# Performance work log

Hardware: AMD Instinct MI355X
Metric: run time of the kernel (lower is better)

Reference implementation:

```python
import jax, jax.numpy as jnp
import numpy as np

N_NODES = 50000
N_EDGES = 800000
DIM = 128
HEADS = 2
DEPTH = 2
MLP = 512
NEG_SLOPE = 0.2  # PyG GATv2 default
EPS = 1e-5


def setup_inputs() -> dict:
    key = jax.random.key(0)
    ks = jax.random.split(key, 10)
    s = 0.05
    p = lambda k, shape: (jax.random.normal(k, shape, jnp.float32) * s)
    x = jax.random.normal(ks[0], (N_NODES, DIM), jnp.float32)
    edge_index = jax.random.randint(ks[1], (2, N_EDGES), 0, N_NODES, dtype=jnp.int64)
    D, H = DEPTH, HEADS
    return {
        "x": x,
        "edge_index": edge_index,
        # per-layer stacked params (leading dim = depth)
        "ln1_g": jnp.ones((D, DIM), jnp.float32), "ln1_b": jnp.zeros((D, DIM), jnp.float32),
        "Wl": p(ks[2], (D, DIM, H * DIM)), "bl": jnp.zeros((D, H * DIM), jnp.float32),
        "Wr": p(ks[3], (D, DIM, H * DIM)), "br": jnp.zeros((D, H * DIM), jnp.float32),
        "att": p(ks[4], (D, H, DIM)),
        "gat_b": jnp.zeros((D, H * DIM), jnp.float32),
        "proj_W": p(ks[5], (D, H * DIM, DIM)), "proj_b": jnp.zeros((D, DIM), jnp.float32),
        "ln2_g": jnp.ones((D, DIM), jnp.float32), "ln2_b": jnp.zeros((D, DIM), jnp.float32),
        "W1": p(ks[6], (D, DIM, MLP)), "b1": jnp.zeros((D, MLP), jnp.float32),
        "W2": p(ks[7], (D, MLP, DIM)), "b2": jnp.zeros((D, DIM), jnp.float32),
    }


def _layer_norm(x, g, b):
    m = jnp.mean(x, axis=-1, keepdims=True)
    v = jnp.var(x, axis=-1, keepdims=True)
    return (x - m) * jax.lax.rsqrt(v + EPS) * g + b


def _gatv2(x, src, dst, Wl, bl, Wr, br, att, gat_b):
    # GATv2Conv: e_ij = att^T LeakyReLU(Wl x_j + Wr x_i); alpha = segment-softmax over dst
    n = x.shape[0]
    xl = (x @ Wl + bl).reshape(n, HEADS, DIM)  # source transform [N,H,D]
    xr = (x @ Wr + br).reshape(n, HEADS, DIM)  # target transform [N,H,D]
    e = jax.nn.leaky_relu(xl[src] + xr[dst], NEG_SLOPE)      # [E,H,D]
    score = jnp.einsum('ehd,hd->eh', e, att)                 # [E,H]
    smax = jax.ops.segment_max(score, dst, num_segments=n)   # [N,H]
    ex = jnp.exp(score - smax[dst])
    denom = jax.ops.segment_sum(ex, dst, num_segments=n)     # [N,H]
    alpha = ex / (denom[dst] + 1e-16)                        # [E,H]
    msg = xl[src] * alpha[..., None]                         # [E,H,D]
    out = jax.ops.segment_sum(msg, dst, num_segments=n)      # [N,H,D]
    return out.reshape(n, HEADS * DIM) + gat_b


def reference(x, edge_index, ln1_g, ln1_b, Wl, bl, Wr, br, att, gat_b,
              proj_W, proj_b, ln2_g, ln2_b, W1, b1, W2, b2):
    src, dst = edge_index[0], edge_index[1]
    for i in range(DEPTH):
        h = _layer_norm(x, ln1_g[i], ln1_b[i])               # PreNorm
        g = _gatv2(h, src, dst, Wl[i], bl[i], Wr[i], br[i], att[i], gat_b[i])
        x = x + (g @ proj_W[i] + proj_b[i])                  # QuickFix proj + Residual
        h = _layer_norm(x, ln2_g[i], ln2_b[i])
        x = x + (jax.nn.gelu(h @ W1[i] + b1[i]) @ W2[i] + b2[i])  # FFN + Residual
    return x
```

## Files before the change

### kernel.cpp

```cpp
#include <hip/hip_runtime.h>

typedef unsigned int uint;
typedef unsigned short ushort;
typedef __attribute__((ext_vector_type(4))) float f32x4;
typedef __attribute__((ext_vector_type(2))) float f32x2;
typedef __attribute__((ext_vector_type(8))) short bf16x8;
typedef _Float16 f16x2 __attribute__((ext_vector_type(2)));

#define N_NODES 50000
#define DIM 128
#define HEADS 2
#define HD 256
#define MLP 512
#define DEPTH 2
#define CAP 96

__device__ __forceinline__ uint f2bf(float f) {
    uint u = __float_as_uint(f);
    return (u + 0x7FFFu + ((u >> 16) & 1u)) >> 16;
}
__device__ __forceinline__ ushort f2h(float f) {
    union { _Float16 h; ushort u; } v;
    v.h = (_Float16)f;
    return v.u;
}
__device__ __forceinline__ f16x2 u2h(uint u) {
    union { uint u; f16x2 h; } v;
    v.u = u;
    return v.h;
}

#if __has_builtin(__builtin_amdgcn_fdot2)
#define FDOT2(a, b, c) __builtin_amdgcn_fdot2((a), (b), (c), false)
#else
#define FDOT2(a, b, c) fmaf((float)(a)[0], (float)(b)[0], fmaf((float)(a)[1], (float)(b)[1], (c)))
#endif
#if __has_builtin(__builtin_amdgcn_exp2f)
#define EXP2F(x) __builtin_amdgcn_exp2f(x)
#else
#define EXP2F(x) exp2f(x)
#endif

__device__ __forceinline__ float gelu_tanh(float x) {
    float t = 0.7978845608028654f * (x + 0.044715f * x * x * x);
    float e = __expf(2.0f * t);
    float th = 1.0f - 2.0f / (e + 1.0f);
    return 0.5f * x * (1.0f + th);
}

__global__ __launch_bounds__(256) void ln_kernel(
    const float* __restrict__ x, const float* __restrict__ g,
    const float* __restrict__ b, ushort* __restrict__ out, int N)
{
    int node = blockIdx.x * 4 + (threadIdx.x >> 6);
    if (node >= N) return;
    int lane = threadIdx.x & 63;
    const float2 v = *(const float2*)(x + (size_t)node * DIM + lane * 2);
    float s = v.x + v.y;
    float s2 = v.x * v.x + v.y * v.y;
    #pragma unroll
    for (int m = 1; m <= 32; m <<= 1) {
        s  += __shfl_xor(s,  m, 64);
        s2 += __shfl_xor(s2, m, 64);
    }
    float mean = s * (1.0f / 128.0f);
    float var  = s2 * (1.0f / 128.0f) - mean * mean;
    float rs = rsqrtf(var + 1e-5f);
    float ox = (v.x - mean) * rs * g[lane * 2]     + b[lane * 2];
    float oy = (v.y - mean) * rs * g[lane * 2 + 1] + b[lane * 2 + 1];
    uint pk = f2bf(ox) | (f2bf(oy) << 16);
    *(uint*)(out + (size_t)node * DIM + lane * 2) = pk;
}

__global__ __launch_bounds__(256) void wconv_all(
    const float* __restrict__ Wl, const float* __restrict__ Wr,
    const float* __restrict__ pW, const float* __restrict__ W1,
    const float* __restrict__ W2, ushort* __restrict__ WlWr_t,
    ushort* __restrict__ pW_t, ushort* __restrict__ W1_t,
    ushort* __restrict__ W2_t)
{
    int i = blockIdx.x * 256 + threadIdx.x;
    if (i < 65536) {
        int l = i >> 15, rem = i & 32767;
        int k = rem >> 8, m = rem & 255;
        WlWr_t[l * 65536 + m * 128 + k] = (ushort)f2bf(Wl[i]);
    } else if (i < 131072) {
        int j = i - 65536;
        int l = j >> 15, rem = j & 32767;
        int k = rem >> 8, m = rem & 255;
        WlWr_t[l * 65536 + (m + 256) * 128 + k] = (ushort)f2bf(Wr[j]);
    } else if (i < 196608) {
        int j = i - 131072;
        int l = j >> 15, rem = j & 32767;
        int k = rem >> 7, m = rem & 127;
        pW_t[l * 32768 + m * 256 + k] = (ushort)f2bf(pW[j]);
    } else if (i < 327680) {
        int j = i - 196608;
        int l = j >> 16, rem = j & 65535;
        int k = rem >> 9, m = rem & 511;
        W1_t[l * 65536 + m * 128 + k] = (ushort)f2bf(W1[j]);
    } else if (i < 458752) {
        int j = i - 327680;
        int l = j >> 16, rem = j & 65535;
        int k = rem >> 7, m = rem & 127;
        W2_t[l * 65536 + m * 512 + k] = (ushort)f2bf(W2[j]);
    }
}

template<int EPI>
__global__ __launch_bounds__(256) void gemm_mfma(
    const ushort* __restrict__ A, const ushort* __restrict__ Bt,
    const float* __restrict__ bias, const float* __restrict__ bias2, int bsplit,
    void* __restrict__ Cout, int Nr, int K, int M)
{
    __shared__ ushort As[128 * 72];
    __shared__ ushort Bs[64 * 72];
    const int tid = threadIdx.x;
    const int wave = tid >> 6, lane = tid & 63;
    const int wm = wave >> 1, wn = wave & 1;
    const int r0 = blockIdx.y * 128;
    const int c0 = blockIdx.x * 64;
    const int l15 = lane & 15, q = lane >> 4;

    f32x4 acc[4][2];
    #pragma unroll
    for (int t = 0; t < 4; ++t)
        #pragma unroll
        for (int u = 0; u < 2; ++u) {
            f32x4 z = {0.f, 0.f, 0.f, 0.f};
            acc[t][u] = z;
        }

    for (int k0 = 0; k0 < K; k0 += 64) {
        #pragma unroll
        for (int p = 0; p < 4; ++p) {
            int flat = p * 256 + tid;
            int row = flat >> 3, c8 = flat & 7;
            int gr = r0 + row; gr = gr < Nr ? gr : Nr - 1;
            uint4 v = *(const uint4*)(A + (size_t)gr * K + k0 + c8 * 8);
            *(uint4*)(As + row * 72 + c8 * 8) = v;
        }
        #pragma unroll
        for (int p = 0; p < 2; ++p) {
            int flat = p * 256 + tid;
            int row = flat >> 3, c8 = flat & 7;
            uint4 v = *(const uint4*)(Bt + (size_t)(c0 + row) * K + k0 + c8 * 8);
            *(uint4*)(Bs + row * 72 + c8 * 8) = v;
        }
        __syncthreads();
        #pragma unroll
        for (int kh = 0; kh < 2; ++kh) {
            const int ko = kh * 32 + q * 8;
            bf16x8 a[4], b[2];
            #pragma unroll
            for (int t = 0; t < 4; ++t)
                a[t] = *(const bf16x8*)(As + (wm * 64 + t * 16 + l15) * 72 + ko);
            #pragma unroll
            for (int u = 0; u < 2; ++u)
                b[u] = *(const bf16x8*)(Bs + (wn * 32 + u * 16 + l15) * 72 + ko);
            #pragma unroll
            for (int t = 0; t < 4; ++t)
                #pragma unroll
                for (int u = 0; u < 2; ++u)
                    acc[t][u] = __builtin_amdgcn_mfma_f32_16x16x32_bf16(
                        a[t], b[u], acc[t][u], 0, 0, 0);
        }
        __syncthreads();
    }

    #pragma unroll
    for (int t = 0; t < 4; ++t) {
        int grow = r0 + wm * 64 + t * 16 + q * 4;
        #pragma unroll
        for (int u = 0; u < 2; ++u) {
            int gcol = c0 + wn * 32 + u * 16 + l15;
            float bv = (gcol < bsplit) ? bias[gcol] : bias2[gcol - bsplit];
            #pragma unroll
            for (int i = 0; i < 4; ++i) {
                int r = grow + i;
                if (r >= Nr) continue;
                float v = acc[t][u][i] + bv;
                if (EPI == 1) v = gelu_tanh(v);
                if (EPI == 0) {
                    ((ushort*)Cout)[(size_t)r * M + gcol] = f2h(v);
                } else {
                    ((ushort*)Cout)[(size_t)r * M + gcol] = (ushort)f2bf(v);
                }
            }
        }
    }
}

__global__ __launch_bounds__(256) void gemm_ln(
    const ushort* __restrict__ A, const ushort* __restrict__ Bt,
    const float* __restrict__ bias, const float* __restrict__ R,
    float* __restrict__ X, const float* __restrict__ lng,
    const float* __restrict__ lnb, ushort* __restrict__ H,
    int Nr, int K)
{
    __shared__ ushort As[64 * 72];
    __shared__ ushort Bs[128 * 72];
    __shared__ float4 part[64];
    const int tid = threadIdx.x;
    const int wave = tid >> 6, lane = tid & 63;
    const int wm = wave >> 1, wn = wave & 1;
    const int r0 = blockIdx.y * 64;
    const int l15 = lane & 15, q = lane >> 4;

    f32x4 acc[2][4];
    #pragma unroll
    for (int t = 0; t < 2; ++t)
        #pragma unroll
        for (int u = 0; u < 4; ++u) {
            f32x4 z = {0.f, 0.f, 0.f, 0.f};
            acc[t][u] = z;
        }

    for (int k0 = 0; k0 < K; k0 += 64) {
        #pragma unroll
        for (int p = 0; p < 2; ++p) {
            int flat = p * 256 + tid;
            int row = flat >> 3, c8 = flat & 7;
            int gr = r0 + row; gr = gr < Nr ? gr : Nr - 1;
            uint4 v = *(const uint4*)(A + (size_t)gr * K + k0 + c8 * 8);
            *(uint4*)(As + row * 72 + c8 * 8) = v;
        }
        #pragma unroll
        for (int p = 0; p < 4; ++p) {
            int flat = p * 256 + tid;
            int row = flat >> 3, c8 = flat & 7;
            uint4 v = *(const uint4*)(Bt + (size_t)row * K + k0 + c8 * 8);
            *(uint4*)(Bs + row * 72 + c8 * 8) = v;
        }
        __syncthreads();
        #pragma unroll
        for (int kh = 0; kh < 2; ++kh) {
            const int ko = kh * 32 + q * 8;
            bf16x8 a[2], b[4];
            #pragma unroll
            for (int t = 0; t < 2; ++t)
                a[t] = *(const bf16x8*)(As + (wm * 32 + t * 16 + l15) * 72 + ko);
            #pragma unroll
            for (int u = 0; u < 4; ++u)
                b[u] = *(const bf16x8*)(Bs + (wn * 64 + u * 16 + l15) * 72 + ko);
            #pragma unroll
            for (int t = 0; t < 2; ++t)
                #pragma unroll
                for (int u = 0; u < 4; ++u)
                    acc[t][u] = __builtin_amdgcn_mfma_f32_16x16x32_bf16(
                        a[t], b[u], acc[t][u], 0, 0, 0);
        }
        __syncthreads();
    }

    float bv[4];
    #pragma unroll
    for (int u = 0; u < 4; ++u) bv[u] = bias[wn * 64 + u * 16 + l15];

    #pragma unroll
    for (int t = 0; t < 2; ++t) {
        #pragma unroll
        for (int i = 0; i < 4; ++i) {
            const int rl = wm * 32 + t * 16 + q * 4 + i;
            const int r = r0 + rl;
            const bool ok = r < Nr;
            float ss = 0.f, ss2 = 0.f;
            #pragma unroll
            for (int u = 0; u < 4; ++u) {
                const int col = wn * 64 + u * 16 + l15;
                float v = acc[t][u][i] + bv[u];
                if (ok) v += R[(size_t)r * DIM + col];
                acc[t][u][i] = v;
                ss += v; ss2 += v * v;
            }
            #pragma unroll
            for (int m = 1; m <= 8; m <<= 1) {
                ss  += __shfl_xor(ss,  m, 64);
                ss2 += __shfl_xor(ss2, m, 64);
            }
            if (ok) {
                #pragma unroll
                for (int u = 0; u < 4; ++u)
                    X[(size_t)r * DIM + wn * 64 + u * 16 + l15] = acc[t][u][i];
            }
            if (l15 == 0) {
                float2 w = { ss, ss2 };
                *(float2*)((float*)&part[rl] + wn * 2) = w;
            }
        }
    }

    if (H != nullptr) {
        __syncthreads();
        float lgv[4], lbv[4];
        #pragma unroll
        for (int u = 0; u < 4; ++u) {
            lgv[u] = lng[wn * 64 + u * 16 + l15];
            lbv[u] = lnb[wn * 64 + u * 16 + l15];
        }
        #pragma unroll
        for (int t = 0; t < 2; ++t) {
            #pragma unroll
            for (int i = 0; i < 4; ++i) {
                const int rl = wm * 32 + t * 16 + q * 4 + i;
                const int r = r0 + rl;
                if (r >= Nr) continue;
                const float4 pp = part[rl];
                const float mean = (pp.x + pp.z) * (1.0f / 128.0f);
                const float var  = (pp.y + pp.w) * (1.0f / 128.0f) - mean * mean;
                const float rs = rsqrtf(var + 1e-5f);
                #pragma unroll
                for (int u = 0; u < 4; ++u) {
                    const int col = wn * 64 + u * 16 + l15;
                    const float hv = (acc[t][u][i] - mean) * rs * lgv[u] + lbv[u];
                    H[(size_t)r * DIM + col] = (ushort)f2bf(hv);
                }
            }
        }
    }
}

__global__ __launch_bounds__(256) void bucket_kernel(
    const int* __restrict__ src, const int* __restrict__ dst,
    int* __restrict__ deg, ushort* __restrict__ esrc, int E)
{
    int e = blockIdx.x * 256 + threadIdx.x;
    if (e >= E) return;
    int d = dst[e];
    int pos = atomicAdd(&deg[d], 1);
    if (pos < CAP) esrc[(size_t)d * CAP + pos] = (ushort)src[e];
}

__global__ __launch_bounds__(256) void gat_gather(
    const int* __restrict__ deg, const ushort* __restrict__ esrc,
    const ushort* __restrict__ xlr, const float* __restrict__ att,
    const float* __restrict__ gat_b, ushort* __restrict__ agg, int N)
{
    int node = blockIdx.x * 4 + (threadIdx.x >> 6);
    if (node >= N) return;
    const int lane = threadIdx.x & 63;
    const int half = lane >> 5, sl = lane & 31;
    const int c = sl * 8;

    const uint4 rq = *(const uint4*)(xlr + (size_t)node * 512 + 256 + c);
    const f16x2 r01 = u2h(rq.x), r23 = u2h(rq.y);
    const f16x2 r45 = u2h(rq.z), r67 = u2h(rq.w);

    const float LOG2E = 1.4426950408889634f;
    const float4 af0 = *(const float4*)(att + c);
    const float4 af1 = *(const float4*)(att + c + 4);
    f16x2 a01, a23, a45, a67;
    a01[0] = (_Float16)(af0.x * LOG2E); a01[1] = (_Float16)(af0.y * LOG2E);
    a23[0] = (_Float16)(af0.z * LOG2E); a23[1] = (_Float16)(af0.w * LOG2E);
    a45[0] = (_Float16)(af1.x * LOG2E); a45[1] = (_Float16)(af1.y * LOG2E);
    a67[0] = (_Float16)(af1.z * LOG2E); a67[1] = (_Float16)(af1.w * LOG2E);
    const f16x2 k02 = { (_Float16)0.2f, (_Float16)0.2f };

    int dc = deg[node]; dc = dc < CAP ? dc : CAP;
    const int base = node * CAP;
    f32x2 acc01 = {0.f, 0.f}, acc23 = {0.f, 0.f}, acc45 = {0.f, 0.f}, acc67 = {0.f, 0.f};
    float den = 0.f;

    if (dc > 0) {
        int slc = sl < dc ? sl : dc - 1;
        const int idxreg = esrc[base + slc];

        auto getsrc = [&](int e) -> int {
            int idx = e < dc ? e : dc - 1;
            int s = __shfl(idxreg, (lane & 32) | (idx & 31), 64);
            if (idx >= 32) s = esrc[base + idx];
            return s;
        };

        const int iters = (dc + 1) >> 1;
        int e0 = half;
        int s0 = getsrc(e0);
        uint4 lq0 = *(const uint4*)(xlr + (size_t)s0 * 512 + c);
        int e1 = e0 + 2;
        int s1 = getsrc(e1);
        uint4 lq1 = *(const uint4*)(xlr + (size_t)s1 * 512 + c);

        for (int it = 0; it < iters; ++it) {
            const int e2 = e0 + 4;
            const int s2 = getsrc(e2);
            const uint4 lq2 = *(const uint4*)(xlr + (size_t)s2 * 512 + c);

            const f16x2 l01 = u2h(lq0.x), l23 = u2h(lq0.y);
            const f16x2 l45 = u2h(lq0.z), l67 = u2h(lq0.w);
            f16x2 t, lr;
            float p = 0.f;
            t = l01 + r01; lr = __builtin_elementwise_max(t, t * k02); p = FDOT2(a01, lr, p);
            t = l23 + r23; lr = __builtin_elementwise_max(t, t * k02); p = FDOT2(a23, lr, p);
            t = l45 + r45; lr = __builtin_elementwise_max(t, t * k02); p = FDOT2(a45, lr, p);
            t = l67 + r67; lr = __builtin_elementwise_max(t, t * k02); p = FDOT2(a67, lr, p);
            p += __shfl_xor(p, 1, 64);
            p += __shfl_xor(p, 2, 64);
            p += __shfl_xor(p, 4, 64);
            p += __shfl_xor(p, 8, 64);
            const float ex = (e0 < dc) ? EXP2F(p) : 0.f;
            acc01.x = fmaf(ex, (float)l01[0], acc01.x);
            acc01.y = fmaf(ex, (float)l01[1], acc01.y);
            acc23.x = fmaf(ex, (float)l23[0], acc23.x);
            acc23.y = fmaf(ex, (float)l23[1], acc23.y);
            acc45.x = fmaf(ex, (float)l45[0], acc45.x);
            acc45.y = fmaf(ex, (float)l45[1], acc45.y);
            acc67.x = fmaf(ex, (float)l67[0], acc67.x);
            acc67.y = fmaf(ex, (float)l67[1], acc67.y);
            den += ex;
            e0 = e1; lq0 = lq1;
            e1 = e2; lq1 = lq2;
        }
    }
    acc01.x += __shfl_xor(acc01.x, 32, 64); acc01.y += __shfl_xor(acc01.y, 32, 64);
    acc23.x += __shfl_xor(acc23.x, 32, 64); acc23.y += __shfl_xor(acc23.y, 32, 64);
    acc45.x += __shfl_xor(acc45.x, 32, 64); acc45.y += __shfl_xor(acc45.y, 32, 64);
    acc67.x += __shfl_xor(acc67.x, 32, 64); acc67.y += __shfl_xor(acc67.y, 32, 64);
    den     += __shfl_xor(den,     32, 64);

    if (half == 0) {
        const float inv = 1.0f / (den + 1e-16f);
        const float4 g0 = *(const float4*)(gat_b + c);
        const float4 g1 = *(const float4*)(gat_b + c + 4);
        uint4 o;
        o.x = f2bf(acc01.x * inv + g0.x) | (f2bf(acc01.y * inv + g0.y) << 16);
        o.y = f2bf(acc23.x * inv + g0.z) | (f2bf(acc23.y * inv + g0.w) << 16);
        o.z = f2bf(acc45.x * inv + g1.x) | (f2bf(acc45.y * inv + g1.y) << 16);
        o.w = f2bf(acc67.x * inv + g1.z) | (f2bf(acc67.y * inv + g1.w) << 16);
        *(uint4*)(agg + (size_t)node * HD + c) = o;
    }
}

extern "C" void kernel_launch(void* const* d_in, const int* in_sizes, int n_in,
                              void* d_out, int out_size, void* d_ws, size_t ws_size,
                              hipStream_t stream) {
    const float* x_in   = (const float*)d_in[0];
    const int*   eidx   = (const int*)d_in[1];
    const float* ln1_g  = (const float*)d_in[2];
    const float* ln1_b  = (const float*)d_in[3];
    const float* Wl     = (const float*)d_in[4];
    const float* bl     = (const float*)d_in[5];
    const float* Wr     = (const float*)d_in[6];
    const float* br     = (const float*)d_in[7];
    const float* att    = (const float*)d_in[8];
    const float* gat_b  = (const float*)d_in[9];
    const float* projW  = (const float*)d_in[10];
    const float* projb  = (const float*)d_in[11];
    const float* ln2_g  = (const float*)d_in[12];
    const float* ln2_b  = (const float*)d_in[13];
    const float* W1     = (const float*)d_in[14];
    const float* b1     = (const float*)d_in[15];
    const float* W2     = (const float*)d_in[16];
    const float* b2     = (const float*)d_in[17];

    const int N = N_NODES;
    const int E = in_sizes[1] / 2;
    const int* src = eidx;
    const int* dst = eidx + E;

    char* ws = (char*)d_ws;
    size_t off = 0;
    ushort* xlr  = (ushort*)(ws + off); off += (size_t)N * 512 * 2;
    ushort* agg  = (ushort*)(ws + off); off += (size_t)N * HD * 2;
    ushort* h    = (ushort*)(ws + off); off += (size_t)N * DIM * 2;
    ushort* WlWr_t = (ushort*)(ws + off); off += (size_t)DEPTH * 512 * 128 * 2;
    ushort* pW_t   = (ushort*)(ws + off); off += (size_t)DEPTH * 128 * 256 * 2;
    ushort* W1_t   = (ushort*)(ws + off); off += (size_t)DEPTH * 512 * 128 * 2;
    ushort* W2_t   = (ushort*)(ws + off); off += (size_t)DEPTH * 128 * 512 * 2;
    int* deg     = (int*)(ws + off);    off += (size_t)N * 4;
    ushort* esrc = (ushort*)(ws + off); off += (size_t)N * CAP * 2;
    ushort* mid  = xlr;

    float* x = (float*)d_out;

    const int nodeBlocks = (N + 3) / 4;
    const dim3 blk(256);
    const int gy128 = (N + 127) / 128;
    const int gy64  = (N + 63) / 64;

    wconv_all<<<(458752 + 255) / 256, blk, 0, stream>>>(
        Wl, Wr, projW, W1, W2, WlWr_t, pW_t, W1_t, W2_t);

    hipMemsetAsync(deg, 0, (size_t)N * 4, stream);
    bucket_kernel<<<(E + 255) / 256, blk, 0, stream>>>(src, dst, deg, esrc, E);

    for (int L = 0; L < DEPTH; ++L) {
        const float* bl_i   = bl + (size_t)L * HD;
        const float* br_i   = br + (size_t)L * HD;
        const float* att_i  = att + (size_t)L * HD;
        const float* gatb_i = gat_b + (size_t)L * HD;
        const float* pb_i   = projb + (size_t)L * DIM;
        const float* b1_i   = b1 + (size_t)L * MLP;
        const float* b2_i   = b2 + (size_t)L * DIM;
        const float* xin_L  = (L == 0) ? x_in : x;

        if (L == 0)
            ln_kernel<<<nodeBlocks, blk, 0, stream>>>(
                x_in, ln1_g, ln1_b, h, N);

        gemm_mfma<0><<<dim3(8, gy128), blk, 0, stream>>>(
            h, WlWr_t + (size_t)L * 512 * 128, bl_i, br_i, HD, xlr, N, 128, 512);
        gat_gather<<<nodeBlocks, blk, 0, stream>>>(deg, esrc, xlr, att_i, gatb_i, agg, N);
        gemm_ln<<<dim3(1, gy64), blk, 0, stream>>>(
            agg, pW_t + (size_t)L * 128 * 256, pb_i, xin_L, x,
            ln2_g + (size_t)L * DIM, ln2_b + (size_t)L * DIM, h, N, 256);
        gemm_mfma<1><<<dim3(8, gy128), blk, 0, stream>>>(
            h, W1_t + (size_t)L * 512 * 128, b1_i, b1_i, 1 << 30, mid, N, 128, 512);
        const bool last = (L + 1 == DEPTH);
        gemm_ln<<<dim3(1, gy64), blk, 0, stream>>>(
            mid, W2_t + (size_t)L * 128 * 512, b2_i, x, x,
            last ? nullptr : ln1_g + (size_t)(L + 1) * DIM,
            last ? nullptr : ln1_b + (size_t)(L + 1) * DIM,
            last ? nullptr : h, N, 512);
    }
}
```

Measured before the change: 540.3 us.

## Fuse FFN up-projection, GELU and down-projection into one kernel

Replaces the separate W1 GEMM (writing a 512-wide bf16 intermediate to global memory) and the W2 GEMM+LN kernel with a single kernel. It keeps each 32-row tile's GELU output in shared memory and feeds it straight into the second MFMA GEMM, then does the residual and the next LayerNorm. W2 is stored with its K index permuted so the packed-pair layout in shared memory lines up with MFMA operand order. The goal is to drop the intermediate global write and read plus one launch. In exchange, weights are read directly from global memory per block without LDS staging, and each block carries a larger shared-memory footprint.

```diff
diff --git a/kernel.cpp b/kernel.cpp
--- a/kernel.cpp
+++ b/kernel.cpp
@@ -103,7 +103,11 @@
         int j = i - 327680;
         int l = j >> 16, rem = j & 65535;
         int k = rem >> 7, m = rem & 127;
-        W2_t[l * 65536 + m * 512 + k] = (ushort)f2bf(W2[j]);
+        int nc = k >> 6, r64 = k & 63;
+        int w = r64 >> 5, r32 = r64 & 31;
+        int hf = r32 >> 4, lo = r32 & 15;
+        int ks = nc * 64 + ((w * 16 + lo) << 1) + hf;
+        W2_t[l * 65536 + m * 512 + ks] = (ushort)f2bf(W2[j]);
     }
 }
 
@@ -315,6 +319,137 @@
                     const float hv = (acc[t][u][i] - mean) * rs * lgv[u] + lbv[u];
                     H[(size_t)r * DIM + col] = (ushort)f2bf(hv);
                 }
+            }
+        }
+    }
+}
+
+__global__ __launch_bounds__(256) void ffn_fused(
+    const ushort* __restrict__ h, const ushort* __restrict__ W1t,
+    const ushort* __restrict__ W2tp, const float* __restrict__ b1,
+    const float* __restrict__ b2, const float* __restrict__ R,
+    float* __restrict__ X, const float* __restrict__ lng,
+    const float* __restrict__ lnb, ushort* __restrict__ H, int Nr)
+{
+    __shared__ ushort As[32 * 140];
+    __shared__ uint  mid[32 * 259];
+    __shared__ float4 part[32];
+    const int tid = threadIdx.x;
+    const int wave = tid >> 6, lane = tid & 63;
+    const int wm = wave >> 1, wn = wave & 1;
+    const int l15 = lane & 15, q = lane >> 4;
+    const int r0 = blockIdx.x * 32;
+
+    #pragma unroll
+    for (int p = 0; p < 2; ++p) {
+        int f = p * 256 + tid;
+        int row = f >> 4, c8 = f & 15;
+        int gr = r0 + row; gr = gr < Nr ? gr : Nr - 1;
+        uint4 v = *(const uint4*)(h + (size_t)gr * DIM + c8 * 8);
+        *(uint4*)(As + row * 140 + c8 * 8) = v;
+    }
+    __syncthreads();
+
+    bf16x8 af[4];
+    #pragma unroll
+    for (int ks = 0; ks < 4; ++ks)
+        af[ks] = *(const bf16x8*)(As + (wm * 16 + l15) * 140 + ks * 32 + q * 8);
+
+    #pragma unroll
+    for (int nc = 0; nc < 8; ++nc) {
+        f32x4 pa[2];
+        #pragma unroll
+        for (int u = 0; u < 2; ++u) { f32x4 z = {0.f,0.f,0.f,0.f}; pa[u] = z; }
+        #pragma unroll
+        for (int u = 0; u < 2; ++u) {
+            const ushort* bp = W1t + (size_t)(nc * 64 + wn * 32 + u * 16 + l15) * 128 + q * 8;
+            #pragma unroll
+            for (int ks = 0; ks < 4; ++ks) {
+                bf16x8 b = *(const bf16x8*)(bp + ks * 32);
+                pa[u] = __builtin_amdgcn_mfma_f32_16x16x32_bf16(af[ks], b, pa[u], 0, 0, 0);
+            }
+        }
+        const float bv0 = b1[nc * 64 + wn * 32 + l15];
+        const float bv1 = b1[nc * 64 + wn * 32 + 16 + l15];
+        #pragma unroll
+        for (int i = 0; i < 4; ++i) {
+            float v0 = gelu_tanh(pa[0][i] + bv0);
+            float v1 = gelu_tanh(pa[1][i] + bv1);
+            mid[(wm * 16 + q * 4 + i) * 259 + nc * 32 + wn * 16 + l15] =
+                f2bf(v0) | (f2bf(v1) << 16);
+        }
+    }
+    __syncthreads();
+
+    f32x4 acc[4];
+    #pragma unroll
+    for (int u = 0; u < 4; ++u) { f32x4 z = {0.f,0.f,0.f,0.f}; acc[u] = z; }
+    #pragma unroll
+    for (int ks = 0; ks < 16; ++ks) {
+        bf16x8 a = *(const bf16x8*)(mid + (wm * 16 + l15) * 259 + ks * 16 + q * 4);
+        #pragma unroll
+        for (int u = 0; u < 4; ++u) {
+            bf16x8 b = *(const bf16x8*)(W2tp + (size_t)(wn * 64 + u * 16 + l15) * 512 + ks * 32 + q * 8);
+            acc[u] = __builtin_amdgcn_mfma_f32_16x16x32_bf16(a, b, acc[u], 0, 0, 0);
+        }
+    }
+
+    float bvv[4];
+    #pragma unroll
+    for (int u = 0; u < 4; ++u) bvv[u] = b2[wn * 64 + u * 16 + l15];
+
+    #pragma unroll
+    for (int i = 0; i < 4; ++i) {
+        const int rl = wm * 16 + q * 4 + i;
+        const int r = r0 + rl;
+        const bool ok = r < Nr;
+        float ss = 0.f, ss2 = 0.f;
+        #pragma unroll
+        for (int u = 0; u < 4; ++u) {
+            const int col = wn * 64 + u * 16 + l15;
+            float v = acc[u][i] + bvv[u];
+            if (ok) v += R[(size_t)r * DIM + col];
+            acc[u][i] = v;
+            ss += v; ss2 += v * v;
+        }
+        #pragma unroll
+        for (int m = 1; m <= 8; m <<= 1) {
+            ss  += __shfl_xor(ss,  m, 64);
+            ss2 += __shfl_xor(ss2, m, 64);
+        }
+        if (ok) {
+            #pragma unroll
+            for (int u = 0; u < 4; ++u)
+                X[(size_t)r * DIM + wn * 64 + u * 16 + l15] = acc[u][i];
+        }
+        if (l15 == 0) {
+            float2 w = { ss, ss2 };
+            *(float2*)((float*)&part[rl] + wn * 2) = w;
+        }
+    }
+
+    if (H != nullptr) {
+        __syncthreads();
+        float lgv[4], lbv[4];
+        #pragma unroll
+        for (int u = 0; u < 4; ++u) {
+            lgv[u] = lng[wn * 64 + u * 16 + l15];
+            lbv[u] = lnb[wn * 64 + u * 16 + l15];
+        }
+        #pragma unroll
+        for (int i = 0; i < 4; ++i) {
+            const int rl = wm * 16 + q * 4 + i;
+            const int r = r0 + rl;
+            if (r >= Nr) continue;
+            const float4 pp = part[rl];
+            const float mean = (pp.x + pp.z) * (1.0f / 128.0f);
+            const float var  = (pp.y + pp.w) * (1.0f / 128.0f) - mean * mean;
+            const float rs = rsqrtf(var + 1e-5f);
+            #pragma unroll
+            for (int u = 0; u < 4; ++u) {
+                const int col = wn * 64 + u * 16 + l15;
+                const float hv = (acc[u][i] - mean) * rs * lgv[u] + lbv[u];
+                H[(size_t)r * DIM + col] = (ushort)f2bf(hv);
             }
         }
     }
@@ -468,7 +603,6 @@
     ushort* W2_t   = (ushort*)(ws + off); off += (size_t)DEPTH * 128 * 512 * 2;
     int* deg     = (int*)(ws + off);    off += (size_t)N * 4;
     ushort* esrc = (ushort*)(ws + off); off += (size_t)N * CAP * 2;
-    ushort* mid  = xlr;
 
     float* x = (float*)d_out;
 
@@ -476,6 +610,7 @@
     const dim3 blk(256);
     const int gy128 = (N + 127) / 128;
     const int gy64  = (N + 63) / 64;
+    const int gyF   = (N + 31) / 32;
 
     wconv_all<<<(458752 + 255) / 256, blk, 0, stream>>>(
         Wl, Wr, projW, W1, W2, WlWr_t, pW_t, W1_t, W2_t);
@@ -503,13 +638,12 @@
         gemm_ln<<<dim3(1, gy64), blk, 0, stream>>>(
             agg, pW_t + (size_t)L * 128 * 256, pb_i, xin_L, x,
             ln2_g + (size_t)L * DIM, ln2_b + (size_t)L * DIM, h, N, 256);
-        gemm_mfma<1><<<dim3(8, gy128), blk, 0, stream>>>(
-            h, W1_t + (size_t)L * 512 * 128, b1_i, b1_i, 1 << 30, mid, N, 128, 512);
         const bool last = (L + 1 == DEPTH);
-        gemm_ln<<<dim3(1, gy64), blk, 0, stream>>>(
-            mid, W2_t + (size_t)L * 128 * 512, b2_i, x, x,
+        ffn_fused<<<dim3(gyF), blk, 0, stream>>>(
+            h, W1_t + (size_t)L * 65536, W2_t + (size_t)L * 65536,
+            b1_i, b2_i, x, x,
             last ? nullptr : ln1_g + (size_t)(L + 1) * DIM,
             last ? nullptr : ln1_b + (size_t)(L + 1) * DIM,
-            last ? nullptr : h, N, 512);
-    }
-}
+            last ? nullptr : h, N);
+    }
+}
```

New measurement: 625.4 us. 1.16x slower.

## Restructure K=128 GEMMs to keep A rows in registers and sweep output columns

Applied to the files above, without the earlier changes.

Replaces the tiled GEMM (128x64 output tiles, A and B staged per K-chunk in shared memory) with a kernel where each block owns 64 rows, loads the whole K=128 A slice once into registers, and loops over the 8 column tiles of the 512-wide output. B tiles are double-buffered in shared memory so the next tile's load overlaps the current MFMAs. This removes the 8x redundant reads of the A matrix and the LDS staging of A. The trade-offs are fewer blocks (one per 64 rows), more registers per thread, and hardcoded K=128/M=512.

```diff
diff --git a/kernel.cpp b/kernel.cpp
--- a/kernel.cpp
+++ b/kernel.cpp
@@ -108,86 +108,86 @@
 }
 
 template<int EPI>
-__global__ __launch_bounds__(256) void gemm_mfma(
+__global__ __launch_bounds__(256) void gemm_fat(
     const ushort* __restrict__ A, const ushort* __restrict__ Bt,
     const float* __restrict__ bias, const float* __restrict__ bias2, int bsplit,
-    void* __restrict__ Cout, int Nr, int K, int M)
+    ushort* __restrict__ Cout, int Nr)
 {
-    __shared__ ushort As[128 * 72];
-    __shared__ ushort Bs[64 * 72];
+    __shared__ ushort Bs[2][64 * 136];
     const int tid = threadIdx.x;
     const int wave = tid >> 6, lane = tid & 63;
     const int wm = wave >> 1, wn = wave & 1;
-    const int r0 = blockIdx.y * 128;
-    const int c0 = blockIdx.x * 64;
+    const int r0 = blockIdx.x * 64;
     const int l15 = lane & 15, q = lane >> 4;
 
-    f32x4 acc[4][2];
+    bf16x8 af[2][4];
     #pragma unroll
-    for (int t = 0; t < 4; ++t)
-        #pragma unroll
-        for (int u = 0; u < 2; ++u) {
-            f32x4 z = {0.f, 0.f, 0.f, 0.f};
-            acc[t][u] = z;
-        }
-
-    for (int k0 = 0; k0 < K; k0 += 64) {
+    for (int t = 0; t < 2; ++t) {
+        int gr = r0 + wm * 32 + t * 16 + l15; gr = gr < Nr ? gr : Nr - 1;
+        #pragma unroll
+        for (int ks = 0; ks < 4; ++ks)
+            af[t][ks] = *(const bf16x8*)(A + (size_t)gr * 128 + ks * 32 + q * 8);
+    }
+
+    auto stageB = [&](int buf, int ct) {
         #pragma unroll
         for (int p = 0; p < 4; ++p) {
             int flat = p * 256 + tid;
-            int row = flat >> 3, c8 = flat & 7;
-            int gr = r0 + row; gr = gr < Nr ? gr : Nr - 1;
-            uint4 v = *(const uint4*)(A + (size_t)gr * K + k0 + c8 * 8);
-            *(uint4*)(As + row * 72 + c8 * 8) = v;
-        }
-        #pragma unroll
-        for (int p = 0; p < 2; ++p) {
-            int flat = p * 256 + tid;
-            int row = flat >> 3, c8 = flat & 7;
-            uint4 v = *(const uint4*)(Bt + (size_t)(c0 + row) * K + k0 + c8 * 8);
-            *(uint4*)(Bs + row * 72 + c8 * 8) = v;
-        }
-        __syncthreads();
-        #pragma unroll
-        for (int kh = 0; kh < 2; ++kh) {
-            const int ko = kh * 32 + q * 8;
-            bf16x8 a[4], b[2];
-            #pragma unroll
-            for (int t = 0; t < 4; ++t)
-                a[t] = *(const bf16x8*)(As + (wm * 64 + t * 16 + l15) * 72 + ko);
+            int row = flat >> 4, c8 = flat & 15;
+            uint4 v = *(const uint4*)(Bt + (size_t)(ct * 64 + row) * 128 + c8 * 8);
+            *(uint4*)(Bs[buf] + row * 136 + c8 * 8) = v;
+        }
+    };
+
+    stageB(0, 0);
+    __syncthreads();
+
+    #pragma unroll
+    for (int ct = 0; ct < 8; ++ct) {
+        const int cur = ct & 1;
+        if (ct < 7) stageB(cur ^ 1, ct + 1);
+
+        f32x4 acc[2][2];
+        #pragma unroll
+        for (int t = 0; t < 2; ++t)
+            #pragma unroll
+            for (int u = 0; u < 2; ++u) {
+                f32x4 z = {0.f, 0.f, 0.f, 0.f};
+                acc[t][u] = z;
+            }
+
+        #pragma unroll
+        for (int ks = 0; ks < 4; ++ks) {
+            bf16x8 b[2];
             #pragma unroll
             for (int u = 0; u < 2; ++u)
-                b[u] = *(const bf16x8*)(Bs + (wn * 32 + u * 16 + l15) * 72 + ko);
-            #pragma unroll
-            for (int t = 0; t < 4; ++t)
+                b[u] = *(const bf16x8*)(Bs[cur] + (wn * 32 + u * 16 + l15) * 136 + ks * 32 + q * 8);
+            #pragma unroll
+            for (int t = 0; t < 2; ++t)
                 #pragma unroll
                 for (int u = 0; u < 2; ++u)
                     acc[t][u] = __builtin_amdgcn_mfma_f32_16x16x32_bf16(
-                        a[t], b[u], acc[t][u], 0, 0, 0);
+                        af[t][ks], b[u], acc[t][u], 0, 0, 0);
+        }
+
+        #pragma unroll
+        for (int t = 0; t < 2; ++t) {
+            int grow = r0 + wm * 32 + t * 16 + q * 4;
+            #pragma unroll
+            for (int u = 0; u < 2; ++u) {
+                int gcol = ct * 64 + wn * 32 + u * 16 + l15;
+                float bv = (gcol < bsplit) ? bias[gcol] : bias2[gcol - bsplit];
+                #pragma unroll
+                for (int i = 0; i < 4; ++i) {
+                    int r = grow + i;
+                    if (r >= Nr) continue;
+                    float v = acc[t][u][i] + bv;
+                    if (EPI == 1) v = gelu_tanh(v);
+                    Cout[(size_t)r * 512 + gcol] = (EPI == 0) ? f2h(v) : (ushort)f2bf(v);
+                }
+            }
         }
         __syncthreads();
-    }
-
-    #pragma unroll
-    for (int t = 0; t < 4; ++t) {
-        int grow = r0 + wm * 64 + t * 16 + q * 4;
-        #pragma unroll
-        for (int u = 0; u < 2; ++u) {
-            int gcol = c0 + wn * 32 + u * 16 + l15;
-            float bv = (gcol < bsplit) ? bias[gcol] : bias2[gcol - bsplit];
-            #pragma unroll
-            for (int i = 0; i < 4; ++i) {
-                int r = grow + i;
-                if (r >= Nr) continue;
-                float v = acc[t][u][i] + bv;
-                if (EPI == 1) v = gelu_tanh(v);
-                if (EPI == 0) {
-                    ((ushort*)Cout)[(size_t)r * M + gcol] = f2h(v);
-                } else {
-                    ((ushort*)Cout)[(size_t)r * M + gcol] = (ushort)f2bf(v);
-                }
-            }
-        }
     }
 }
 
@@ -474,7 +474,6 @@
 
     const int nodeBlocks = (N + 3) / 4;
     const dim3 blk(256);
-    const int gy128 = (N + 127) / 128;
     const int gy64  = (N + 63) / 64;
 
     wconv_all<<<(458752 + 255) / 256, blk, 0, stream>>>(
@@ -497,17 +496,17 @@
             ln_kernel<<<nodeBlocks, blk, 0, stream>>>(
                 x_in, ln1_g, ln1_b, h, N);
 
-        gemm_mfma<0><<<dim3(8, gy128), blk, 0, stream>>>(
-            h, WlWr_t + (size_t)L * 512 * 128, bl_i, br_i, HD, xlr, N, 128, 512);
+        gemm_fat<0><<<dim3(gy64), blk, 0, stream>>>(
+            h, WlWr_t + (size_t)L * 65536, bl_i, br_i, HD, xlr, N);
         gat_gather<<<nodeBlocks, blk, 0, stream>>>(deg, esrc, xlr, att_i, gatb_i, agg, N);
         gemm_ln<<<dim3(1, gy64), blk, 0, stream>>>(
             agg, pW_t + (size_t)L * 128 * 256, pb_i, xin_L, x,
             ln2_g + (size_t)L * DIM, ln2_b + (size_t)L * DIM, h, N, 256);
-        gemm_mfma<1><<<dim3(8, gy128), blk, 0, stream>>>(
-            h, W1_t + (size_t)L * 512 * 128, b1_i, b1_i, 1 << 30, mid, N, 128, 512);
+        gemm_fat<1><<<dim3(gy64), blk, 0, stream>>>(
+            h, W1_t + (size_t)L * 65536, b1_i, b1_i, 1 << 30, mid, N);
         const bool last = (L + 1 == DEPTH);
         gemm_ln<<<dim3(1, gy64), blk, 0, stream>>>(
-            mid, W2_t + (size_t)L * 128 * 512, b2_i, x, x,
+            mid, W2_t + (size_t)L * 65536, b2_i, x, x,
             last ? nullptr : ln1_g + (size_t)(L + 1) * DIM,
             last ? nullptr : ln1_b + (size_t)(L + 1) * DIM,
             last ? nullptr : h, N, 512);
```

Result: no change. 547.6 us (+1.3%).
